# Optimization experiments

Measured on AMD Instinct MI355X. Metric: run time of the kernel, lower is better.

The kernel has to match this reference:

```python
import jax, jax.numpy as jnp
import numpy as np

M, N, D, B = 8192, 64, 1, 25

# ---- quaternion / dual-quaternion algebra (w, x, y, z convention) ----

def qmul(a, b):
    aw, av = a[..., :1], a[..., 1:]
    bw, bv = b[..., :1], b[..., 1:]
    w = aw * bw - jnp.sum(av * bv, -1, keepdims=True)
    v = aw * bv + bw * av + jnp.cross(av, bv)
    return jnp.concatenate([w, v], -1)

def qconj(q):
    return q * jnp.array([1.0, -1.0, -1.0, -1.0], q.dtype)

def qrotate(q, v):
    w, qv = q[..., :1], q[..., 1:]
    uv = jnp.cross(qv, v)
    return v + 2.0 * (w * uv + jnp.cross(qv, uv))

def dq_inverse(dq):
    return (qconj(dq[0]), qconj(dq[1]))

def dq_mul(a, b):
    return (qmul(a[0], b[0]), qmul(a[0], b[1]) + qmul(a[1], b[0]))

def dq_apply(dq, pts):
    qr, qd = dq
    t = 2.0 * qmul(qd, qconj(qr))[..., 1:]  # translation part
    return qrotate(qr, pts) + t


def setup_inputs() -> dict:
    key = jax.random.key(0)
    ks = jax.random.split(key, 4)

    def make_dq(k, pre):
        k1, k2 = jax.random.split(k)
        qr = jax.random.normal(k1, pre + (4,), jnp.float32)
        qr = qr / jnp.linalg.norm(qr, axis=-1, keepdims=True)
        t = 0.2 * jax.random.normal(k2, pre + (3,), jnp.float32)
        tq = jnp.concatenate([jnp.zeros(pre + (1,), jnp.float32), t], -1)
        return qr, 0.5 * qmul(tq, qr)  # unit dual quaternion

    xyz = 0.3 * jax.random.normal(ks[0], (M, N, D, 3), jnp.float32)
    t_qr, t_qd = make_dq(ks[1], (M, B))
    r_qr, r_qd = make_dq(ks[2], (1, B))  # rest pose shared across frames, then expanded
    rest_qr = jnp.broadcast_to(r_qr, (M, B, 4))
    rest_qd = jnp.broadcast_to(r_qd, (M, B, 4))
    log_gauss = jnp.log(0.03) * jnp.ones((B, 3), jnp.float32) \
        + 0.1 * jax.random.normal(ks[3], (B, 3), jnp.float32)
    return {"xyz": xyz, "t_qr": t_qr, "t_qd": t_qd,
            "rest_qr": rest_qr, "rest_qd": rest_qd, "log_gauss": log_gauss}


def reference(xyz, t_qr, t_qd, rest_qr, rest_qd, log_gauss):
    # type == 'forward': se3 maps rest pose -> time-t pose
    t_art = (t_qr, t_qd)
    rest_art = (rest_qr, rest_qd)
    se3 = dq_mul(t_art, dq_inverse(rest_art))  # ((M,B,4),(M,B,4))

    # SkinningField: Gaussian bone influence in rest-bone coordinates
    art = (rest_qr[:, None, None], rest_qd[:, None, None])  # (M,1,1,B,4)
    xyz_bone = dq_apply(dq_inverse(art), xyz[..., None, :])  # (M,N,D,B,3)
    scale = jnp.exp(log_gauss)  # (B,3) per-bone anisotropic gauss scale
    dist2 = jnp.sum((xyz_bone / scale) ** 2, -1)  # (M,N,D,B)
    skin_prob = jax.nn.softmax(-0.5 * dist2, -1)  # softmax over bones

    # dual-quaternion blend skinning: sign-align to first bone, blend, normalize
    sign = jnp.sign(jnp.sum(se3[0] * se3[0][:, :1], -1, keepdims=True))
    sign = jnp.where(sign == 0, 1.0, sign)
    qr_s, qd_s = se3[0] * sign, se3[1] * sign
    qr_b = jnp.einsum('mndb,mbk->mndk', skin_prob, qr_s)  # (M,N,D,4)
    qd_b = jnp.einsum('mndb,mbk->mndk', skin_prob, qd_s)
    norm = jnp.linalg.norm(qr_b, axis=-1, keepdims=True)
    out = dq_apply((qr_b / norm, qd_b / norm), xyz)  # (M,N,D,3)
    return out
```

## Files before the change

### kernel.cpp

```cpp
#include <hip/hip_runtime.h>
#include <math.h>

#define MM 8192
#define NN 64
#define NB 25
#define WAVES 4

struct Q { float w, x, y, z; };

__device__ __forceinline__ Q qmul(const Q a, const Q b) {
    Q r;
    r.w = a.w*b.w - a.x*b.x - a.y*b.y - a.z*b.z;
    r.x = a.w*b.x + b.w*a.x + a.y*b.z - a.z*b.y;
    r.y = a.w*b.y + b.w*a.y + a.z*b.x - a.x*b.z;
    r.z = a.w*b.z + b.w*a.z + a.x*b.y - a.y*b.x;
    return r;
}

__global__ __launch_bounds__(WAVES*64) void skin_kernel(
    const float* __restrict__ xyz,
    const float* __restrict__ t_qr,
    const float* __restrict__ t_qd,
    const float* __restrict__ rest_qr,
    const float* __restrict__ rest_qd,
    const float* __restrict__ log_gauss,
    float* __restrict__ out)
{
    __shared__ float s_mat[WAVES][NB][12];
    __shared__ float s_qr[WAVES][NB][4];
    __shared__ float s_qd[WAVES][NB][4];
    __shared__ float s_is[NB][3];

    const int wave = threadIdx.x >> 6;
    const int lane = threadIdx.x & 63;
    const int m = blockIdx.x * WAVES + wave;

    if (threadIdx.x < NB * 3) {
        s_is[threadIdx.x / 3][threadIdx.x % 3] = __expf(-log_gauss[threadIdx.x]);
    }
    __syncthreads();

    if (lane < NB) {
        const int base = (m * NB + lane) * 4;
        const float4 Tqv = *reinterpret_cast<const float4*>(t_qr + base);
        const float4 Tdv = *reinterpret_cast<const float4*>(t_qd + base);
        const float4 Rqv = *reinterpret_cast<const float4*>(rest_qr + base);
        const float4 Rdv = *reinterpret_cast<const float4*>(rest_qd + base);
        const Q Tq{Tqv.x, Tqv.y, Tqv.z, Tqv.w};
        const Q Td{Tdv.x, Tdv.y, Tdv.z, Tdv.w};
        const Q Rq{Rqv.x, Rqv.y, Rqv.z, Rqv.w};
        const Q Rd{Rdv.x, Rdv.y, Rdv.z, Rdv.w};
        const Q Rqc{Rq.w, -Rq.x, -Rq.y, -Rq.z};
        const Q Rdc{Rd.w, -Rd.x, -Rd.y, -Rd.z};

        const Q se_r = qmul(Tq, Rqc);
        const Q m1 = qmul(Tq, Rdc);
        const Q m2 = qmul(Td, Rqc);
        const Q se_d{m1.w + m2.w, m1.x + m2.x, m1.y + m2.y, m1.z + m2.z};

        const float d0 = se_r.w * __shfl(se_r.w, 0)
                       + se_r.x * __shfl(se_r.x, 0)
                       + se_r.y * __shfl(se_r.y, 0)
                       + se_r.z * __shfl(se_r.z, 0);
        const float sg = (d0 < 0.f) ? -1.f : 1.f;

        s_qr[wave][lane][0] = sg * se_r.w;
        s_qr[wave][lane][1] = sg * se_r.x;
        s_qr[wave][lane][2] = sg * se_r.y;
        s_qr[wave][lane][3] = sg * se_r.z;
        s_qd[wave][lane][0] = sg * se_d.w;
        s_qd[wave][lane][1] = sg * se_d.x;
        s_qd[wave][lane][2] = sg * se_d.y;
        s_qd[wave][lane][3] = sg * se_d.z;

        const Q tq = qmul(Rdc, Rq);
        const float tbx = 2.f * tq.x, tby = 2.f * tq.y, tbz = 2.f * tq.z;

        const float qw = Rqc.w, qx = Rqc.x, qy = Rqc.y, qz = Rqc.z;
        const float r00 = 1.f - 2.f*(qy*qy + qz*qz), r01 = 2.f*(qx*qy - qw*qz), r02 = 2.f*(qx*qz + qw*qy);
        const float r10 = 2.f*(qx*qy + qw*qz), r11 = 1.f - 2.f*(qx*qx + qz*qz), r12 = 2.f*(qy*qz - qw*qx);
        const float r20 = 2.f*(qx*qz - qw*qy), r21 = 2.f*(qy*qz + qw*qx), r22 = 1.f - 2.f*(qx*qx + qy*qy);
        const float i0 = s_is[lane][0], i1 = s_is[lane][1], i2 = s_is[lane][2];
        float* mp = s_mat[wave][lane];
        mp[0] = r00*i0; mp[1]  = r01*i0; mp[2]  = r02*i0; mp[3]  = tbx*i0;
        mp[4] = r10*i1; mp[5]  = r11*i1; mp[6]  = r12*i1; mp[7]  = tby*i1;
        mp[8] = r20*i2; mp[9]  = r21*i2; mp[10] = r22*i2; mp[11] = tbz*i2;
    }
    __syncthreads();

    const int pbase = (m * NN + lane) * 3;
    const float px = xyz[pbase], py = xyz[pbase + 1], pz = xyz[pbase + 2];

    float logit[NB];
    float mx = -1e30f;
#pragma unroll
    for (int b = 0; b < NB; ++b) {
        const float* mp = s_mat[wave][b];
        const float vx = fmaf(mp[0], px, fmaf(mp[1],  py, fmaf(mp[2],  pz, mp[3])));
        const float vy = fmaf(mp[4], px, fmaf(mp[5],  py, fmaf(mp[6],  pz, mp[7])));
        const float vz = fmaf(mp[8], px, fmaf(mp[9],  py, fmaf(mp[10], pz, mp[11])));
        const float lg = -0.5f * (vx*vx + vy*vy + vz*vz);
        logit[b] = lg;
        mx = fmaxf(mx, lg);
    }

    float aw = 0.f, ax = 0.f, ay = 0.f, az = 0.f;
    float bw = 0.f, bx = 0.f, by = 0.f, bz = 0.f;
#pragma unroll
    for (int b = 0; b < NB; ++b) {
        const float e = __expf(logit[b] - mx);
        aw = fmaf(e, s_qr[wave][b][0], aw);
        ax = fmaf(e, s_qr[wave][b][1], ax);
        ay = fmaf(e, s_qr[wave][b][2], ay);
        az = fmaf(e, s_qr[wave][b][3], az);
        bw = fmaf(e, s_qd[wave][b][0], bw);
        bx = fmaf(e, s_qd[wave][b][1], bx);
        by = fmaf(e, s_qd[wave][b][2], by);
        bz = fmaf(e, s_qd[wave][b][3], bz);
    }

    const float inv = rsqrtf(aw*aw + ax*ax + ay*ay + az*az);
    const Q qr{aw*inv, ax*inv, ay*inv, az*inv};
    const Q qd{bw*inv, bx*inv, by*inv, bz*inv};
    const Q qrc{qr.w, -qr.x, -qr.y, -qr.z};
    const Q tq = qmul(qd, qrc);

    const float uvx = qr.y*pz - qr.z*py;
    const float uvy = qr.z*px - qr.x*pz;
    const float uvz = qr.x*py - qr.y*px;
    const float cx = qr.y*uvz - qr.z*uvy;
    const float cy = qr.z*uvx - qr.x*uvz;
    const float cz = qr.x*uvy - qr.y*uvx;

    out[pbase]     = px + 2.f*(qr.w*uvx + cx) + 2.f*tq.x;
    out[pbase + 1] = py + 2.f*(qr.w*uvy + cy) + 2.f*tq.y;
    out[pbase + 2] = pz + 2.f*(qr.w*uvz + cz) + 2.f*tq.z;
}

extern "C" void kernel_launch(void* const* d_in, const int* in_sizes, int n_in,
                              void* d_out, int out_size, void* d_ws, size_t ws_size,
                              hipStream_t stream) {
    const float* xyz      = (const float*)d_in[0];
    const float* t_qr     = (const float*)d_in[1];
    const float* t_qd     = (const float*)d_in[2];
    const float* rest_qr  = (const float*)d_in[3];
    const float* rest_qd  = (const float*)d_in[4];
    const float* log_gauss= (const float*)d_in[5];
    float* out = (float*)d_out;

    dim3 grid(MM / WAVES);
    dim3 block(WAVES * 64);
    hipLaunchKernelGGL(skin_kernel, grid, block, 0, stream,
                       xyz, t_qr, t_qd, rest_qr, rest_qd, log_gauss, out);
}
```

Measured before the change: 18.98 us.

## Replace LDS bone tables with readlane broadcasts and quadratic-form logits

Drops the shared-memory bone tables and both block barriers. Each lane now computes its bone's data in registers, and the other lanes fetch it with scalar readlane broadcasts. The per-bone squared Mahalanobis distance is expanded into a 10-coefficient quadratic form in the point coordinates, which cuts per-bone logit work from about 12 FMAs plus squares to 9 FMAs. The trade-offs are many readlane (SGPR) operations and possible cancellation error from the expanded quadratic form.

```diff
diff --git a/kernel.cpp b/kernel.cpp
--- a/kernel.cpp
+++ b/kernel.cpp
@@ -5,6 +5,13 @@
 #define NN 64
 #define NB 25
 #define WAVES 4
+
+__device__ __forceinline__ float rl(float x, int b) {
+    return __int_as_float(__builtin_amdgcn_readlane(__float_as_int(x), b));
+}
+__device__ __forceinline__ float rfl(float x) {
+    return __int_as_float(__builtin_amdgcn_readfirstlane(__float_as_int(x)));
+}
 
 struct Q { float w, x, y, z; };
 
@@ -26,82 +33,81 @@
     const float* __restrict__ log_gauss,
     float* __restrict__ out)
 {
-    __shared__ float s_mat[WAVES][NB][12];
-    __shared__ float s_qr[WAVES][NB][4];
-    __shared__ float s_qd[WAVES][NB][4];
-    __shared__ float s_is[NB][3];
-
     const int wave = threadIdx.x >> 6;
     const int lane = threadIdx.x & 63;
     const int m = blockIdx.x * WAVES + wave;
+    const int bl = (lane < NB) ? lane : (NB - 1);
 
-    if (threadIdx.x < NB * 3) {
-        s_is[threadIdx.x / 3][threadIdx.x % 3] = __expf(-log_gauss[threadIdx.x]);
-    }
-    __syncthreads();
+    const int qbase = (m * NB + bl) * 4;
+    const float4 Tqv = *reinterpret_cast<const float4*>(t_qr + qbase);
+    const float4 Tdv = *reinterpret_cast<const float4*>(t_qd + qbase);
+    const float4 Rqv = *reinterpret_cast<const float4*>(rest_qr + qbase);
+    const float4 Rdv = *reinterpret_cast<const float4*>(rest_qd + qbase);
+    const float i0 = __expf(-log_gauss[bl * 3 + 0]);
+    const float i1 = __expf(-log_gauss[bl * 3 + 1]);
+    const float i2 = __expf(-log_gauss[bl * 3 + 2]);
 
-    if (lane < NB) {
-        const int base = (m * NB + lane) * 4;
-        const float4 Tqv = *reinterpret_cast<const float4*>(t_qr + base);
-        const float4 Tdv = *reinterpret_cast<const float4*>(t_qd + base);
-        const float4 Rqv = *reinterpret_cast<const float4*>(rest_qr + base);
-        const float4 Rdv = *reinterpret_cast<const float4*>(rest_qd + base);
-        const Q Tq{Tqv.x, Tqv.y, Tqv.z, Tqv.w};
-        const Q Td{Tdv.x, Tdv.y, Tdv.z, Tdv.w};
-        const Q Rq{Rqv.x, Rqv.y, Rqv.z, Rqv.w};
-        const Q Rd{Rdv.x, Rdv.y, Rdv.z, Rdv.w};
-        const Q Rqc{Rq.w, -Rq.x, -Rq.y, -Rq.z};
-        const Q Rdc{Rd.w, -Rd.x, -Rd.y, -Rd.z};
+    const Q Tq{Tqv.x, Tqv.y, Tqv.z, Tqv.w};
+    const Q Td{Tdv.x, Tdv.y, Tdv.z, Tdv.w};
+    const Q Rq{Rqv.x, Rqv.y, Rqv.z, Rqv.w};
+    const Q Rqc{Rq.w, -Rq.x, -Rq.y, -Rq.z};
+    const Q Rdc{Rdv.x, -Rdv.y, -Rdv.z, -Rdv.w};
 
-        const Q se_r = qmul(Tq, Rqc);
-        const Q m1 = qmul(Tq, Rdc);
-        const Q m2 = qmul(Td, Rqc);
-        const Q se_d{m1.w + m2.w, m1.x + m2.x, m1.y + m2.y, m1.z + m2.z};
+    const Q se_r = qmul(Tq, Rqc);
+    const Q m1 = qmul(Tq, Rdc);
+    const Q m2 = qmul(Td, Rqc);
+    const Q se_d{m1.w + m2.w, m1.x + m2.x, m1.y + m2.y, m1.z + m2.z};
 
-        const float d0 = se_r.w * __shfl(se_r.w, 0)
-                       + se_r.x * __shfl(se_r.x, 0)
-                       + se_r.y * __shfl(se_r.y, 0)
-                       + se_r.z * __shfl(se_r.z, 0);
-        const float sg = (d0 < 0.f) ? -1.f : 1.f;
+    const float d0 = se_r.w * rfl(se_r.w) + se_r.x * rfl(se_r.x)
+                   + se_r.y * rfl(se_r.y) + se_r.z * rfl(se_r.z);
+    const float sg = (d0 < 0.f) ? -1.f : 1.f;
+    const float qrw = sg * se_r.w, qrx = sg * se_r.x, qry = sg * se_r.y, qrz = sg * se_r.z;
+    const float qdw = sg * se_d.w, qdx = sg * se_d.x, qdy = sg * se_d.y, qdz = sg * se_d.z;
 
-        s_qr[wave][lane][0] = sg * se_r.w;
-        s_qr[wave][lane][1] = sg * se_r.x;
-        s_qr[wave][lane][2] = sg * se_r.y;
-        s_qr[wave][lane][3] = sg * se_r.z;
-        s_qd[wave][lane][0] = sg * se_d.w;
-        s_qd[wave][lane][1] = sg * se_d.x;
-        s_qd[wave][lane][2] = sg * se_d.y;
-        s_qd[wave][lane][3] = sg * se_d.z;
+    const Q tqb = qmul(Rdc, Rq);
+    const float tbx = 2.f * tqb.x, tby = 2.f * tqb.y, tbz = 2.f * tqb.z;
 
-        const Q tq = qmul(Rdc, Rq);
-        const float tbx = 2.f * tq.x, tby = 2.f * tq.y, tbz = 2.f * tq.z;
+    const float qw = Rqc.w, qx = Rqc.x, qy = Rqc.y, qz = Rqc.z;
+    const float r00 = 1.f - 2.f*(qy*qy + qz*qz), r01 = 2.f*(qx*qy - qw*qz), r02 = 2.f*(qx*qz + qw*qy);
+    const float r10 = 2.f*(qx*qy + qw*qz), r11 = 1.f - 2.f*(qx*qx + qz*qz), r12 = 2.f*(qy*qz - qw*qx);
+    const float r20 = 2.f*(qx*qz - qw*qy), r21 = 2.f*(qy*qz + qw*qx), r22 = 1.f - 2.f*(qx*qx + qy*qy);
 
-        const float qw = Rqc.w, qx = Rqc.x, qy = Rqc.y, qz = Rqc.z;
-        const float r00 = 1.f - 2.f*(qy*qy + qz*qz), r01 = 2.f*(qx*qy - qw*qz), r02 = 2.f*(qx*qz + qw*qy);
-        const float r10 = 2.f*(qx*qy + qw*qz), r11 = 1.f - 2.f*(qx*qx + qz*qz), r12 = 2.f*(qy*qz - qw*qx);
-        const float r20 = 2.f*(qx*qz - qw*qy), r21 = 2.f*(qy*qz + qw*qx), r22 = 1.f - 2.f*(qx*qx + qy*qy);
-        const float i0 = s_is[lane][0], i1 = s_is[lane][1], i2 = s_is[lane][2];
-        float* mp = s_mat[wave][lane];
-        mp[0] = r00*i0; mp[1]  = r01*i0; mp[2]  = r02*i0; mp[3]  = tbx*i0;
-        mp[4] = r10*i1; mp[5]  = r11*i1; mp[6]  = r12*i1; mp[7]  = tby*i1;
-        mp[8] = r20*i2; mp[9]  = r21*i2; mp[10] = r22*i2; mp[11] = tbz*i2;
-    }
-    __syncthreads();
+    const float g00 = r00*i0, g01 = r01*i0, g02 = r02*i0;
+    const float g10 = r10*i1, g11 = r11*i1, g12 = r12*i1;
+    const float g20 = r20*i2, g21 = r21*i2, g22 = r22*i2;
+    const float u0 = tbx*i0, u1 = tby*i1, u2 = tbz*i2;
+
+    const float k0 = -0.5f*(g00*g00 + g10*g10 + g20*g20);
+    const float k1 = -0.5f*(g01*g01 + g11*g11 + g21*g21);
+    const float k2 = -0.5f*(g02*g02 + g12*g12 + g22*g22);
+    const float k3 = -(g00*g01 + g10*g11 + g20*g21);
+    const float k4 = -(g00*g02 + g10*g12 + g20*g22);
+    const float k5 = -(g01*g02 + g11*g12 + g21*g22);
+    const float k6 = -(g00*u0 + g10*u1 + g20*u2);
+    const float k7 = -(g01*u0 + g11*u1 + g21*u2);
+    const float k8 = -(g02*u0 + g12*u1 + g22*u2);
+    const float k9 = -0.5f*(u0*u0 + u1*u1 + u2*u2);
 
     const int pbase = (m * NN + lane) * 3;
     const float px = xyz[pbase], py = xyz[pbase + 1], pz = xyz[pbase + 2];
+    const float fxx = px*px, fyy = py*py, fzz = pz*pz;
+    const float fxy = px*py, fxz = px*pz, fyz = py*pz;
 
     float logit[NB];
-    float mx = -1e30f;
+    float mx = -3.4e38f;
 #pragma unroll
     for (int b = 0; b < NB; ++b) {
-        const float* mp = s_mat[wave][b];
-        const float vx = fmaf(mp[0], px, fmaf(mp[1],  py, fmaf(mp[2],  pz, mp[3])));
-        const float vy = fmaf(mp[4], px, fmaf(mp[5],  py, fmaf(mp[6],  pz, mp[7])));
-        const float vz = fmaf(mp[8], px, fmaf(mp[9],  py, fmaf(mp[10], pz, mp[11])));
-        const float lg = -0.5f * (vx*vx + vy*vy + vz*vz);
-        logit[b] = lg;
-        mx = fmaxf(mx, lg);
+        float t = fmaf(rl(k8, b), pz, rl(k9, b));
+        t = fmaf(rl(k7, b), py, t);
+        t = fmaf(rl(k6, b), px, t);
+        t = fmaf(rl(k5, b), fyz, t);
+        t = fmaf(rl(k4, b), fxz, t);
+        t = fmaf(rl(k3, b), fxy, t);
+        t = fmaf(rl(k2, b), fzz, t);
+        t = fmaf(rl(k1, b), fyy, t);
+        t = fmaf(rl(k0, b), fxx, t);
+        logit[b] = t;
+        mx = fmaxf(mx, t);
     }
 
     float aw = 0.f, ax = 0.f, ay = 0.f, az = 0.f;
@@ -109,14 +115,14 @@
 #pragma unroll
     for (int b = 0; b < NB; ++b) {
         const float e = __expf(logit[b] - mx);
-        aw = fmaf(e, s_qr[wave][b][0], aw);
-        ax = fmaf(e, s_qr[wave][b][1], ax);
-        ay = fmaf(e, s_qr[wave][b][2], ay);
-        az = fmaf(e, s_qr[wave][b][3], az);
-        bw = fmaf(e, s_qd[wave][b][0], bw);
-        bx = fmaf(e, s_qd[wave][b][1], bx);
-        by = fmaf(e, s_qd[wave][b][2], by);
-        bz = fmaf(e, s_qd[wave][b][3], bz);
+        aw = fmaf(e, rl(qrw, b), aw);
+        ax = fmaf(e, rl(qrx, b), ax);
+        ay = fmaf(e, rl(qry, b), ay);
+        az = fmaf(e, rl(qrz, b), az);
+        bw = fmaf(e, rl(qdw, b), bw);
+        bx = fmaf(e, rl(qdx, b), bx);
+        by = fmaf(e, rl(qdy, b), by);
+        bz = fmaf(e, rl(qdz, b), bz);
     }
 
     const float inv = rsqrtf(aw*aw + ax*ax + ay*ay + az*az);
@@ -140,12 +146,12 @@
 extern "C" void kernel_launch(void* const* d_in, const int* in_sizes, int n_in,
                               void* d_out, int out_size, void* d_ws, size_t ws_size,
                               hipStream_t stream) {
-    const float* xyz      = (const float*)d_in[0];
-    const float* t_qr     = (const float*)d_in[1];
-    const float* t_qd     = (const float*)d_in[2];
-    const float* rest_qr  = (const float*)d_in[3];
-    const float* rest_qd  = (const float*)d_in[4];
-    const float* log_gauss= (const float*)d_in[5];
+    const float* xyz       = (const float*)d_in[0];
+    const float* t_qr      = (const float*)d_in[1];
+    const float* t_qd      = (const float*)d_in[2];
+    const float* rest_qr   = (const float*)d_in[3];
+    const float* rest_qd   = (const float*)d_in[4];
+    const float* log_gauss = (const float*)d_in[5];
     float* out = (float*)d_out;
 
     dim3 grid(MM / WAVES);
```

Result: slower. 23.51 us (+23.9%).
